# Optimization experiments

Hardware: AMD Instinct MI355X
Metric: run time of the kernel (lower is better)

## Reference

```python
import jax, jax.numpy as jnp
import numpy as np
import math

N_HEADS = 4
N_ITERS = 2  # SSFormer n=2; each loop iteration recomputes the same values (no feedback in the original code)
BN_EPS = 1e-5


def _attention(q, k, v):
    """SSTransformer: multi-head cross-attention over flattened spatial dims.
    q,k,v: [B, C, H, W] -> returns [B, C, L] with L = H*W.
    """
    b, c = q.shape[0], q.shape[1]
    L = q.shape[2] * q.shape[3]
    ch = c // N_HEADS
    scale = 1.0 / math.sqrt(math.sqrt(ch))
    qf = (q.reshape(b * N_HEADS, ch, L) * scale)
    kf = (k.reshape(b * N_HEADS, ch, L) * scale)
    vf = v.reshape(b * N_HEADS, ch, L)
    # weight: [B*H, t, s]
    w = jnp.einsum('bct,bcs->bts', qf, kf)
    w = jax.nn.softmax(w.astype(jnp.float32), axis=-1).astype(w.dtype)
    a = jnp.einsum('bts,bcs->bct', w, vf)
    return a.reshape(b, c, L)


def setup_inputs() -> dict:
    key = jax.random.key(0)
    k1, k2, k3, k4 = jax.random.split(key, 4)
    B, C, H, W = 8, 512, 32, 32
    c = jax.random.normal(k1, (B, C, H, W), dtype=jnp.float32)
    e = jax.random.normal(k2, (B, C, H, W), dtype=jnp.float32)
    conv_w = jax.random.normal(k3, (C, C, 1, 1), dtype=jnp.float32) / math.sqrt(C)
    conv_b = jax.random.normal(k4, (C,), dtype=jnp.float32) * 0.02
    bn_gamma = jnp.ones((C,), dtype=jnp.float32)
    bn_beta = jnp.zeros((C,), dtype=jnp.float32)
    return {"c": c, "e": e, "conv_w": conv_w, "conv_b": conv_b,
            "bn_gamma": bn_gamma, "bn_beta": bn_beta}


def reference(c, e, conv_w, conv_b, bn_gamma, bn_beta):
    bs, ch, h, w = c.shape
    L = h * w
    for _ in range(N_ITERS):
        _c = _attention(e, c, c)                       # [B, C, L]
        _e = _attention(_c.reshape(bs, ch, h, w), e, e)  # [B, C, L]
    _e = _e.reshape(bs, ch, h, w)
    # Proj: 1x1 conv + BatchNorm2d (training-mode batch stats) + Swish
    x = jnp.einsum('oc,bchw->bohw', conv_w.reshape(ch, ch), _e) + conv_b[None, :, None, None]
    mean = jnp.mean(x, axis=(0, 2, 3), keepdims=True)
    var = jnp.var(x, axis=(0, 2, 3), keepdims=True)
    xn = (x - mean) * jax.lax.rsqrt(var + BN_EPS)
    xn = xn * bn_gamma[None, :, None, None] + bn_beta[None, :, None, None]
    return xn * jax.nn.sigmoid(xn)
```

## Files before the change

### kernel.cpp

```cpp
#include <hip/hip_runtime.h>
#include <hip/hip_bf16.h>

typedef __attribute__((ext_vector_type(8))) short short8;
typedef __attribute__((ext_vector_type(4))) float floatx4;
typedef __attribute__((ext_vector_type(4))) float f32x4;
typedef __attribute__((ext_vector_type(16))) float f32x16;
typedef unsigned short u16;
typedef unsigned int u32;
typedef __attribute__((ext_vector_type(4))) unsigned int u32x4;
typedef __attribute__((ext_vector_type(8))) unsigned short ushort8;

#define LSEQ 1024
#define CHD  128
#define CEXP 0.12751744900425577f
#define THR_RAW 62.73318f

static __device__ __forceinline__ float b2f(u16 u) {
  union { u32 i; float f; } x; x.i = ((u32)u) << 16; return x.f;
}
static __device__ __forceinline__ u16 f2b(float f) {
  __hip_bfloat16 h = __float2bfloat16(f);
  return *reinterpret_cast<u16*>(&h);
}
static __device__ __forceinline__ u32 cvtpk(float a, float b) {
  u32 r;
  asm("v_cvt_pk_bf16_f32 %0, %1, %2" : "=v"(r) : "v"(a), "v"(b));
  return r;
}
static __device__ __forceinline__ void swap32(u32& a, u32& b) {
  asm("v_permlane32_swap_b32 %0, %1" : "+v"(a), "+v"(b));
}
static __device__ __forceinline__ short8 mk8(u32 a, u32 b, u32 c, u32 d) {
  union { u32x4 u; short8 s; } x;
  x.u[0] = a; x.u[1] = b; x.u[2] = c; x.u[3] = d;
  return x.s;
}
static __device__ __forceinline__ float exp2f_fast(float x) {
  float r;
  asm("v_exp_f32 %0, %1" : "=v"(r) : "v"(x));
  return r;
}
static __device__ __forceinline__ void gl_lds16(const void* g, void* l) {
  __builtin_amdgcn_global_load_lds((__attribute__((address_space(1))) const void*)g,
                                   (__attribute__((address_space(3))) void*)l, 16, 0, 0);
}
#define BARRIER() do { asm volatile("" ::: "memory"); __builtin_amdgcn_s_barrier(); asm volatile("" ::: "memory"); } while (0)
#define LGKM0()   do { asm volatile("s_waitcnt lgkmcnt(0)" ::: "memory"); __builtin_amdgcn_sched_barrier(0); } while (0)

__global__ __launch_bounds__(256) void k_prep(const float* __restrict__ cin,
                                              const float* __restrict__ ein,
                                              const float* __restrict__ Wf,
                                              u16* __restrict__ cV, u16* __restrict__ cT,
                                              u16* __restrict__ eV, u16* __restrict__ eT,
                                              u16* __restrict__ wb, float* __restrict__ zbuf) {
  __shared__ u16 tile[32][72];
  int z = blockIdx.z;
  int tid = threadIdx.x;
  if (z >= 64) {
    int wblk = (z - 64) * 64 + blockIdx.y * 16 + blockIdx.x;
    int base = (wblk * 256 + tid) * 8;
    f32x4 a = *(const f32x4*)(Wf + base);
    f32x4 b = *(const f32x4*)(Wf + base + 4);
    u32x4 u;
    u[0] = cvtpk(a[0], a[1]); u[1] = cvtpk(a[2], a[3]);
    u[2] = cvtpk(b[0], b[1]); u[3] = cvtpk(b[2], b[3]);
    *(u32x4*)(wb + base) = u;
    if (wblk == 0) {
      f32x4 zz; zz[0]=0.f; zz[1]=0.f; zz[2]=0.f; zz[3]=0.f;
      *(f32x4*)(zbuf + tid * 4) = zz;
    }
    return;
  }
  const float* in = (z < 32) ? cin : ein;
  u16* outV = (z < 32) ? cV : eV;
  u16* outT = (z < 32) ? cT : eT;
  int bh = z & 31, c0 = blockIdx.y * 32, s0 = blockIdx.x * 64;
  int cl = tid >> 3, sc = tid & 7;
  size_t off = ((size_t)bh * CHD + c0 + cl) * LSEQ + s0 + sc * 8;
  f32x4 a = *(const f32x4*)(in + off);
  f32x4 b = *(const f32x4*)(in + off + 4);
  u32x4 u;
  u[0] = cvtpk(a[0], a[1]); u[1] = cvtpk(a[2], a[3]);
  u[2] = cvtpk(b[0], b[1]); u[3] = cvtpk(b[2], b[3]);
  *(u32x4*)(outV + off) = u;
  *(u32x4*)&tile[cl][sc * 8] = u;
  __syncthreads();
  int sl = tid >> 2, cc = tid & 3;
  ushort8 v;
#pragma unroll
  for (int j = 0; j < 8; ++j) v[j] = tile[cc * 8 + j][sl];
  *(ushort8*)(outT + ((size_t)bh * LSEQ + s0 + sl) * CHD + c0 + cc * 8) = v;
}

__global__ __launch_bounds__(256, 2) void k_attn(const u16* __restrict__ eT,
                                                 const u16* __restrict__ cT,
                                                 const u16* __restrict__ cV,
                                                 const u16* __restrict__ eV,
                                                 u16* __restrict__ outT) {
  __shared__ char ldsbuf[66560];

  int bh = blockIdx.x, tt = blockIdx.y;
  int tid = threadIdx.x;
  int w = tid >> 6, lane = tid & 63;
  int tw = w & 1, sw = w >> 1;
  int ln = lane & 31, h = lane >> 5;
  int t0 = tt * 64 + tw * 32;

  float* bmbuf = (float*)(ldsbuf + 65536);
  float* lbuf  = (float*)(ldsbuf + 65536 + 512);

  auto stageK = [&](int buf, int sb, const char* kTb) {
#pragma unroll
    for (int it = 0; it < 4; ++it) {
      int bb = it * 4096 + tid * 16;
      int row = bb >> 8;
      int cb = (bb & 255) ^ ((row & 15) << 4);
      gl_lds16(kTb + (size_t)(sb * 64 + row) * 256 + cb, ldsbuf + buf * 16384 + bb);
    }
  };
  auto stageV = [&](int buf, int sb, const char* vb) {
#pragma unroll
    for (int it = 0; it < 4; ++it) {
      int bb = it * 4096 + tid * 16;
      int row = bb >> 7;
      int cb = (bb & 127) ^ ((row & 7) << 4);
      gl_lds16(vb + (size_t)row * 2048 + sb * 128 + cb, ldsbuf + 32768 + buf * 16384 + bb);
    }
  };

  short8 bq[8];
  f32x16 oacc[4];
  float m_r, l_r;
  int swz = (ln & 7) << 4;
  int kswz = (ln & 15) << 4;
  int krow = sw * 32 + ln;

  auto flash = [&](const char* kTb, const char* vb) {
    m_r = -1e30f; l_r = 0.f;
#pragma unroll
    for (int i = 0; i < 4; ++i)
#pragma unroll
      for (int r = 0; r < 16; ++r) oacc[i][r] = 0.f;

    stageK(0, 0, kTb); stageV(0, 0, vb);
    asm volatile("s_waitcnt vmcnt(0)" ::: "memory");
    BARRIER();

    for (int sb = 0; sb < 16; ++sb) {
      int cur = sb & 1;
      const char* K = ldsbuf + cur * 16384;
      const char* V = ldsbuf + 32768 + cur * 16384;
      f32x16 sa;
#pragma unroll
      for (int r = 0; r < 16; ++r) sa[r] = 0.f;

      if (sb < 15) stageK(cur ^ 1, sb + 1, kTb);
      short8 ka0 = *(const short8*)(K + krow * 256 + ((0  + h * 16) ^ kswz));
      short8 ka1 = *(const short8*)(K + krow * 256 + ((32 + h * 16) ^ kswz));
      short8 ka2 = *(const short8*)(K + krow * 256 + ((64 + h * 16) ^ kswz));
      short8 ka3 = *(const short8*)(K + krow * 256 + ((96 + h * 16) ^ kswz));
      BARRIER();
      LGKM0();
      __builtin_amdgcn_s_setprio(1);
      sa = __builtin_amdgcn_mfma_f32_32x32x16_bf16(ka0, bq[0], sa, 0, 0, 0);
      sa = __builtin_amdgcn_mfma_f32_32x32x16_bf16(ka1, bq[1], sa, 0, 0, 0);
      sa = __builtin_amdgcn_mfma_f32_32x32x16_bf16(ka2, bq[2], sa, 0, 0, 0);
      sa = __builtin_amdgcn_mfma_f32_32x32x16_bf16(ka3, bq[3], sa, 0, 0, 0);
      __builtin_amdgcn_s_setprio(0);
      BARRIER();

      if (sb < 15) stageV(cur ^ 1, sb + 1, vb);
      short8 kb0 = *(const short8*)(K + krow * 256 + ((128 + h * 16) ^ kswz));
      short8 kb1 = *(const short8*)(K + krow * 256 + ((160 + h * 16) ^ kswz));
      short8 kb2 = *(const short8*)(K + krow * 256 + ((192 + h * 16) ^ kswz));
      short8 kb3 = *(const short8*)(K + krow * 256 + ((224 + h * 16) ^ kswz));
      BARRIER();
      LGKM0();
      __builtin_amdgcn_s_setprio(1);
      sa = __builtin_amdgcn_mfma_f32_32x32x16_bf16(kb0, bq[4], sa, 0, 0, 0);
      sa = __builtin_amdgcn_mfma_f32_32x32x16_bf16(kb1, bq[5], sa, 0, 0, 0);
      sa = __builtin_amdgcn_mfma_f32_32x32x16_bf16(kb2, bq[6], sa, 0, 0, 0);
      sa = __builtin_amdgcn_mfma_f32_32x32x16_bf16(kb3, bq[7], sa, 0, 0, 0);
      __builtin_amdgcn_s_setprio(0);
      BARRIER();

      float bm = fmaxf(fmaxf(sa[0], sa[1]), fmaxf(sa[2], sa[3]));
      bm = fmaxf(bm, fmaxf(fmaxf(sa[4], sa[5]), fmaxf(sa[6], sa[7])));
      bm = fmaxf(bm, fmaxf(fmaxf(sa[8], sa[9]), fmaxf(sa[10], sa[11])));
      bm = fmaxf(bm, fmaxf(fmaxf(sa[12], sa[13]), fmaxf(sa[14], sa[15])));
      bm = fmaxf(bm, __shfl_xor(bm, 32));
      if (lane < 32) bmbuf[(tw * 2 + sw) * 32 + lane] = bm;
      LGKM0();
      BARRIER();
      bm = fmaxf(bm, bmbuf[(tw * 2 + (sw ^ 1)) * 32 + ln]);
      bool stay = __all(bm - m_r <= THR_RAW);
      if (!stay) {
        float mn = fmaxf(m_r, bm);
        float corr = exp2f_fast((m_r - mn) * CEXP);
        m_r = mn; l_r *= corr;
#pragma unroll
        for (int i = 0; i < 4; ++i)
#pragma unroll
          for (int r = 0; r < 16; ++r) oacc[i][r] *= corr;
      }
      float mnC = m_r * CEXP;
      float rs = 0.f;
#pragma unroll
      for (int r = 0; r < 16; ++r) {
        float p = exp2f_fast(__builtin_fmaf(sa[r], CEXP, -mnC));
        sa[r] = p; rs += p;
      }
      rs += __shfl_xor(rs, 32);
      l_r += rs;

      short8 bp0, bp1;
      {
        u32 w0 = cvtpk(sa[0], sa[1]),  w1 = cvtpk(sa[2], sa[3]);
        u32 w2 = cvtpk(sa[4], sa[5]),  w3 = cvtpk(sa[6], sa[7]);
        swap32(w0, w2); swap32(w1, w3);
        bp0 = mk8(w0, w1, w2, w3);
        u32 w4 = cvtpk(sa[8], sa[9]),  w5 = cvtpk(sa[10], sa[11]);
        u32 w6 = cvtpk(sa[12], sa[13]), w7 = cvtpk(sa[14], sa[15]);
        swap32(w4, w6); swap32(w5, w7);
        bp1 = mk8(w4, w5, w6, w7);
      }

      int vc0 = sw * 64 + h * 16;
      short8 va0 = *(const short8*)(V + (0  + ln) * 128 + (vc0 ^ swz));
      short8 va1 = *(const short8*)(V + (32 + ln) * 128 + (vc0 ^ swz));
      short8 va2 = *(const short8*)(V + (64 + ln) * 128 + (vc0 ^ swz));
      short8 va3 = *(const short8*)(V + (96 + ln) * 128 + (vc0 ^ swz));
      BARRIER();
      LGKM0();
      __builtin_amdgcn_s_setprio(1);
      oacc[0] = __builtin_amdgcn_mfma_f32_32x32x16_bf16(va0, bp0, oacc[0], 0, 0, 0);
      oacc[1] = __builtin_amdgcn_mfma_f32_32x32x16_bf16(va1, bp0, oacc[1], 0, 0, 0);
      oacc[2] = __builtin_amdgcn_mfma_f32_32x32x16_bf16(va2, bp0, oacc[2], 0, 0, 0);
      oacc[3] = __builtin_amdgcn_mfma_f32_32x32x16_bf16(va3, bp0, oacc[3], 0, 0, 0);
      __builtin_amdgcn_s_setprio(0);
      BARRIER();

      int vc1 = sw * 64 + 32 + h * 16;
      short8 vb0 = *(const short8*)(V + (0  + ln) * 128 + (vc1 ^ swz));
      short8 vb1 = *(const short8*)(V + (32 + ln) * 128 + (vc1 ^ swz));
      short8 vb2 = *(const short8*)(V + (64 + ln) * 128 + (vc1 ^ swz));
      short8 vb3 = *(const short8*)(V + (96 + ln) * 128 + (vc1 ^ swz));
      BARRIER();
      LGKM0();
      __builtin_amdgcn_s_setprio(1);
      oacc[0] = __builtin_amdgcn_mfma_f32_32x32x16_bf16(vb0, bp1, oacc[0], 0, 0, 0);
      oacc[1] = __builtin_amdgcn_mfma_f32_32x32x16_bf16(vb1, bp1, oacc[1], 0, 0, 0);
      oacc[2] = __builtin_amdgcn_mfma_f32_32x32x16_bf16(vb2, bp1, oacc[2], 0, 0, 0);
      oacc[3] = __builtin_amdgcn_mfma_f32_32x32x16_bf16(vb3, bp1, oacc[3], 0, 0, 0);
      __builtin_amdgcn_s_setprio(0);
      asm volatile("s_waitcnt vmcnt(0)" ::: "memory");
      BARRIER();
    }
  };

  auto merge_sw = [&]() {
    float* mb = (float*)(ldsbuf + 32768 + tw * 16384);
    if (sw == 1) {
#pragma unroll
      for (int i = 0; i < 4; ++i)
#pragma unroll
        for (int r = 0; r < 16; ++r) mb[(i * 16 + r) * 64 + lane] = oacc[i][r];
      if (lane < 32) lbuf[tw * 32 + lane] = l_r;
    }
    LGKM0();
    BARRIER();
    if (sw == 0) {
#pragma unroll
      for (int i = 0; i < 4; ++i)
#pragma unroll
        for (int r = 0; r < 16; ++r) oacc[i][r] += mb[(i * 16 + r) * 64 + lane];
      l_r += lbuf[tw * 32 + ln];
    }
  };

  const u16* qbase = eT + ((size_t)bh * LSEQ + t0 + ln) * CHD + h * 8;
#pragma unroll
  for (int k = 0; k < 8; ++k) bq[k] = *(const short8*)(qbase + k * 16);

  flash((const char*)(cT + (size_t)bh * LSEQ * CHD),
        (const char*)(cV + (size_t)bh * CHD * LSEQ));

  merge_sw();
  if (sw == 0) {
    float inv = 1.0f / l_r;
    char* qt = ldsbuf + tw * 8192;
#pragma unroll
    for (int m = 0; m < 4; ++m)
#pragma unroll
      for (int q = 0; q < 8; ++q) {
        u32 pk = cvtpk(oacc[m][2 * q] * inv, oacc[m][2 * q + 1] * inv);
        int c2 = m * 64 + 4 * (q & 1) + 16 * (q >> 1) + 8 * h;
        *(u32*)(qt + ln * 256 + (c2 ^ swz)) = pk;
      }
  }
  LGKM0();
  BARRIER();
  {
    const char* qt = ldsbuf + tw * 8192;
#pragma unroll
    for (int k = 0; k < 8; ++k)
      bq[k] = *(const short8*)(qt + ln * 256 + ((k * 32 + h * 16) ^ swz));
  }
  LGKM0();
  BARRIER();

  flash((const char*)(eT + (size_t)bh * LSEQ * CHD),
        (const char*)(eV + (size_t)bh * CHD * LSEQ));

  merge_sw();
  BARRIER();
  if (sw == 0) {
    float inv = 1.0f / l_r;
    char* ot = ldsbuf + tw * 8192;
#pragma unroll
    for (int m = 0; m < 4; ++m)
#pragma unroll
      for (int q = 0; q < 8; ++q) {
        u32 pk = cvtpk(oacc[m][2 * q] * inv, oacc[m][2 * q + 1] * inv);
        int c2 = m * 64 + 4 * (q & 1) + 16 * (q >> 1) + 8 * h;
        *(u32*)(ot + ln * 256 + (c2 ^ swz)) = pk;
      }
    asm volatile("" ::: "memory");
    u16* orow = outT + ((size_t)bh * LSEQ + t0 + ln) * CHD;
#pragma unroll
    for (int it = 0; it < 8; ++it) {
      int col = h * 128 + it * 16;
      ushort8 d = *(const ushort8*)(ot + ln * 256 + (col ^ swz));
      *(ushort8*)((char*)orow + col) = d;
    }
  }
}

__global__ __launch_bounds__(256) void k_proj(const u16* __restrict__ Wm,
                                              const u16* __restrict__ eT,
                                              const float* __restrict__ bias,
                                              u16* __restrict__ x,
                                              float* __restrict__ chsum,
                                              float* __restrict__ chsq) {
  __shared__ char lds[65536];
  int lt = blockIdx.x, ot = blockIdx.y;
  int b = lt >> 3;
  int l0b = (lt & 7) * 128;
  int o0 = ot * 128;
  int tid = threadIdx.x, w = tid >> 6, lane = tid & 63, lo = lane & 15, hi = lane >> 4;
  int wm = w >> 1, wn = w & 1;
  const char* Wb = (const char*)Wm;
  const char* eTb = (const char*)eT;

  auto stageA = [&](int buf, int kb) {
    char* dst = lds + buf * 16384;
#pragma unroll
    for (int it = 0; it < 4; ++it) {
      int bb = it * 4096 + tid * 16;
      int row = bb >> 7;
      int cb = (bb & 127) ^ ((row & 7) << 4);
      gl_lds16(Wb + (size_t)(o0 + row) * 1024 + kb * 128 + cb, dst + bb);
    }
  };
  auto stageB = [&](int buf, int kb) {
    char* dst = lds + 32768 + buf * 16384;
    int page = b * 4 + (kb >> 1);
    int choff = (kb & 1) * 128;
#pragma unroll
    for (int it = 0; it < 4; ++it) {
      int bb = it * 4096 + tid * 16;
      int row = bb >> 7;
      int cb = (bb & 127) ^ ((row & 7) << 4);
      gl_lds16(eTb + ((size_t)page * 1024 + l0b + row) * 256 + choff + cb, dst + bb);
    }
  };

  floatx4 acc[4][4];
#pragma unroll
  for (int i = 0; i < 4; ++i)
#pragma unroll
    for (int j = 0; j < 4; ++j) { acc[i][j][0]=0.f; acc[i][j][1]=0.f; acc[i][j][2]=0.f; acc[i][j][3]=0.f; }

  stageA(0, 0); stageB(0, 0);

  for (int kb = 0; kb < 8; ++kb) {
    int cur = kb & 1;
    __builtin_amdgcn_s_barrier();
    if (kb < 7) { stageA(cur ^ 1, kb + 1); stageB(cur ^ 1, kb + 1); }
    if (kb < 7) { asm volatile("s_waitcnt vmcnt(8)" ::: "memory"); }
    else        { asm volatile("s_waitcnt vmcnt(0)" ::: "memory"); }
    __builtin_amdgcn_s_barrier();
    const char* A = lds + cur * 16384;
    const char* B = lds + 32768 + cur * 16384;
#pragma unroll
    for (int kk = 0; kk < 2; ++kk) {
      short8 af[4], bf[4];
#pragma unroll
      for (int mi = 0; mi < 4; ++mi) {
        int row = wm * 64 + mi * 16 + lo;
        af[mi] = *(const short8*)(A + row * 128 + ((kk * 64 + hi * 16) ^ ((row & 7) << 4)));
      }
#pragma unroll
      for (int ni = 0; ni < 4; ++ni) {
        int row = wn * 64 + ni * 16 + lo;
        bf[ni] = *(const short8*)(B + row * 128 + ((kk * 64 + hi * 16) ^ ((row & 7) << 4)));
      }
      __builtin_amdgcn_s_setprio(1);
#pragma unroll
      for (int mi = 0; mi < 4; ++mi)
#pragma unroll
        for (int ni = 0; ni < 4; ++ni)
          acc[mi][ni] = __builtin_amdgcn_mfma_f32_16x16x32_bf16(af[mi], bf[ni], acc[mi][ni], 0, 0, 0);
      __builtin_amdgcn_s_setprio(0);
    }
  }

#pragma unroll
  for (int mi = 0; mi < 4; ++mi) {
#pragma unroll
    for (int r = 0; r < 4; ++r) {
      int o = o0 + wm * 64 + mi * 16 + hi * 4 + r;
      float bv = bias[o];
      float s = 0.f, q = 0.f;
#pragma unroll
      for (int ni = 0; ni < 4; ++ni) {
        float xv = acc[mi][ni][r] + bv;
        x[((size_t)b * 512 + o) * LSEQ + l0b + wn * 64 + ni * 16 + lo] = f2b(xv);
        s += xv; q += xv * xv;
      }
#pragma unroll
      for (int d = 1; d < 16; d <<= 1) { s += __shfl_xor(s, d); q += __shfl_xor(q, d); }
      if (lo == 0) {
        atomicAdd(&chsum[o], s);
        atomicAdd(&chsq[o], q);
      }
    }
  }
}

__global__ __launch_bounds__(256) void k_final(const u16* __restrict__ x,
                                               const float* __restrict__ chsum,
                                               const float* __restrict__ chsq,
                                               const float* __restrict__ gamma,
                                               const float* __restrict__ beta,
                                               float* __restrict__ out) {
  int idx = blockIdx.x * 256 + threadIdx.x;
  int base = idx * 8;
  int ch = (base >> 10) & 511;
  const float invn = 1.0f / 8192.0f;
  float mean = chsum[ch] * invn;
  float var = chsq[ch] * invn - mean * mean;
  float rstd = rsqrtf(var + 1e-5f);
  float sc = gamma[ch] * rstd;
  float sh = beta[ch] - mean * sc;
  ushort8 vx = *(const ushort8*)(x + base);
  f32x4 o0, o1;
#pragma unroll
  for (int j = 0; j < 8; ++j) {
    float xn = b2f(vx[j]) * sc + sh;
    float sg = 1.0f / (1.0f + __expf(-xn));
    float r = xn * sg;
    if (j < 4) o0[j] = r; else o1[j - 4] = r;
  }
  *(f32x4*)(out + base) = o0;
  *(f32x4*)(out + base + 4) = o1;
}

extern "C" void kernel_launch(void* const* d_in, const int* in_sizes, int n_in,
                              void* d_out, int out_size, void* d_ws, size_t ws_size,
                              hipStream_t stream) {
  const float* c     = (const float*)d_in[0];
  const float* e     = (const float*)d_in[1];
  const float* Wf    = (const float*)d_in[2];
  const float* bias  = (const float*)d_in[3];
  const float* gamma = (const float*)d_in[4];
  const float* beta  = (const float*)d_in[5];
  float* outp = (float*)d_out;

  char* ws = (char*)d_ws;
  const size_t TB = (size_t)32 * 1024 * 128 * 2;
  u16* eT  = (u16*)(ws);
  u16* cT  = (u16*)(ws + TB);
  u16* cV  = (u16*)(ws + 2 * TB);
  u16* eV  = (u16*)(ws + 3 * TB);
  u16* xT  = (u16*)(ws + 4 * TB);
  u16* Wbf = (u16*)(ws + 5 * TB);
  float* chsum = (float*)(ws + 5 * TB + (1 << 20));
  float* chsq  = chsum + 512;
  u16* x   = (u16*)(ws + 6 * TB);

  dim3 tb(256);

  k_prep<<<dim3(16, 4, 66), tb, 0, stream>>>(c, e, Wf, cV, cT, eV, eT, Wbf, chsum);
  k_attn<<<dim3(32, 16), tb, 0, stream>>>(eT, cT, cV, eV, xT);
  k_proj<<<dim3(64, 4), tb, 0, stream>>>(Wbf, xT, bias, x, chsum, chsq);
  k_final<<<dim3(2048), tb, 0, stream>>>(x, chsum, chsq, gamma, beta, outp);
}
```

Baseline: 106.2 us.

## Decouple split-KV waves with independent softmax max and merge-time rescale

The per-block cross-wave max exchange through LDS is removed. Each s-split wave now keeps its own running max, and the two partial results are merged once at the end with exp-based rescaling. The K/V staging is restructured into one barrier pair per block, prefetching both next tiles together with a partial vmcnt wait. All K and V fragments are loaded up front, and the QK^T MFMA chain is split into two independent accumulators to shorten dependency chains. This removes many barriers per iteration, in exchange for more live registers and a slightly more complex final merge.

```diff
diff --git a/kernel.cpp b/kernel.cpp
--- a/kernel.cpp
+++ b/kernel.cpp
@@ -45,7 +45,7 @@
                                    (__attribute__((address_space(3))) void*)l, 16, 0, 0);
 }
 #define BARRIER() do { asm volatile("" ::: "memory"); __builtin_amdgcn_s_barrier(); asm volatile("" ::: "memory"); } while (0)
-#define LGKM0()   do { asm volatile("s_waitcnt lgkmcnt(0)" ::: "memory"); __builtin_amdgcn_sched_barrier(0); } while (0)
+#define LGKM0()   do { asm volatile("s_waitcnt lgkmcnt(0)" ::: "memory"); } while (0)
 
 __global__ __launch_bounds__(256) void k_prep(const float* __restrict__ cin,
                                               const float* __restrict__ ein,
@@ -106,9 +106,6 @@
   int ln = lane & 31, h = lane >> 5;
   int t0 = tt * 64 + tw * 32;
 
-  float* bmbuf = (float*)(ldsbuf + 65536);
-  float* lbuf  = (float*)(ldsbuf + 65536 + 512);
-
   auto stageK = [&](int buf, int sb, const char* kTb) {
 #pragma unroll
     for (int it = 0; it < 4; ++it) {
@@ -143,56 +140,52 @@
       for (int r = 0; r < 16; ++r) oacc[i][r] = 0.f;
 
     stageK(0, 0, kTb); stageV(0, 0, vb);
-    asm volatile("s_waitcnt vmcnt(0)" ::: "memory");
-    BARRIER();
 
     for (int sb = 0; sb < 16; ++sb) {
       int cur = sb & 1;
+      BARRIER();
+      if (sb < 15) { stageK(cur ^ 1, sb + 1, kTb); stageV(cur ^ 1, sb + 1, vb); }
+      if (sb < 15) { asm volatile("s_waitcnt vmcnt(8)" ::: "memory"); }
+      else         { asm volatile("s_waitcnt vmcnt(0)" ::: "memory"); }
+      BARRIER();
+
       const char* K = ldsbuf + cur * 16384;
       const char* V = ldsbuf + 32768 + cur * 16384;
+
+      short8 kf[8], vf0[4], vf1[4];
+#pragma unroll
+      for (int k = 0; k < 8; ++k)
+        kf[k] = *(const short8*)(K + krow * 256 + ((k * 32 + h * 16) ^ kswz));
+      int vc0 = sw * 64 + h * 16, vc1 = sw * 64 + 32 + h * 16;
+#pragma unroll
+      for (int m = 0; m < 4; ++m) {
+        vf0[m] = *(const short8*)(V + (m * 32 + ln) * 128 + (vc0 ^ swz));
+        vf1[m] = *(const short8*)(V + (m * 32 + ln) * 128 + (vc1 ^ swz));
+      }
+
+      f32x16 saA, saB;
+#pragma unroll
+      for (int r = 0; r < 16; ++r) { saA[r] = 0.f; saB[r] = 0.f; }
+      __builtin_amdgcn_s_setprio(1);
+      saA = __builtin_amdgcn_mfma_f32_32x32x16_bf16(kf[0], bq[0], saA, 0, 0, 0);
+      saB = __builtin_amdgcn_mfma_f32_32x32x16_bf16(kf[4], bq[4], saB, 0, 0, 0);
+      saA = __builtin_amdgcn_mfma_f32_32x32x16_bf16(kf[1], bq[1], saA, 0, 0, 0);
+      saB = __builtin_amdgcn_mfma_f32_32x32x16_bf16(kf[5], bq[5], saB, 0, 0, 0);
+      saA = __builtin_amdgcn_mfma_f32_32x32x16_bf16(kf[2], bq[2], saA, 0, 0, 0);
+      saB = __builtin_amdgcn_mfma_f32_32x32x16_bf16(kf[6], bq[6], saB, 0, 0, 0);
+      saA = __builtin_amdgcn_mfma_f32_32x32x16_bf16(kf[3], bq[3], saA, 0, 0, 0);
+      saB = __builtin_amdgcn_mfma_f32_32x32x16_bf16(kf[7], bq[7], saB, 0, 0, 0);
+      __builtin_amdgcn_s_setprio(0);
+
       f32x16 sa;
 #pragma unroll
-      for (int r = 0; r < 16; ++r) sa[r] = 0.f;
-
-      if (sb < 15) stageK(cur ^ 1, sb + 1, kTb);
-      short8 ka0 = *(const short8*)(K + krow * 256 + ((0  + h * 16) ^ kswz));
-      short8 ka1 = *(const short8*)(K + krow * 256 + ((32 + h * 16) ^ kswz));
-      short8 ka2 = *(const short8*)(K + krow * 256 + ((64 + h * 16) ^ kswz));
-      short8 ka3 = *(const short8*)(K + krow * 256 + ((96 + h * 16) ^ kswz));
-      BARRIER();
-      LGKM0();
-      __builtin_amdgcn_s_setprio(1);
-      sa = __builtin_amdgcn_mfma_f32_32x32x16_bf16(ka0, bq[0], sa, 0, 0, 0);
-      sa = __builtin_amdgcn_mfma_f32_32x32x16_bf16(ka1, bq[1], sa, 0, 0, 0);
-      sa = __builtin_amdgcn_mfma_f32_32x32x16_bf16(ka2, bq[2], sa, 0, 0, 0);
-      sa = __builtin_amdgcn_mfma_f32_32x32x16_bf16(ka3, bq[3], sa, 0, 0, 0);
-      __builtin_amdgcn_s_setprio(0);
-      BARRIER();
-
-      if (sb < 15) stageV(cur ^ 1, sb + 1, vb);
-      short8 kb0 = *(const short8*)(K + krow * 256 + ((128 + h * 16) ^ kswz));
-      short8 kb1 = *(const short8*)(K + krow * 256 + ((160 + h * 16) ^ kswz));
-      short8 kb2 = *(const short8*)(K + krow * 256 + ((192 + h * 16) ^ kswz));
-      short8 kb3 = *(const short8*)(K + krow * 256 + ((224 + h * 16) ^ kswz));
-      BARRIER();
-      LGKM0();
-      __builtin_amdgcn_s_setprio(1);
-      sa = __builtin_amdgcn_mfma_f32_32x32x16_bf16(kb0, bq[4], sa, 0, 0, 0);
-      sa = __builtin_amdgcn_mfma_f32_32x32x16_bf16(kb1, bq[5], sa, 0, 0, 0);
-      sa = __builtin_amdgcn_mfma_f32_32x32x16_bf16(kb2, bq[6], sa, 0, 0, 0);
-      sa = __builtin_amdgcn_mfma_f32_32x32x16_bf16(kb3, bq[7], sa, 0, 0, 0);
-      __builtin_amdgcn_s_setprio(0);
-      BARRIER();
+      for (int r = 0; r < 16; ++r) sa[r] = saA[r] + saB[r];
 
       float bm = fmaxf(fmaxf(sa[0], sa[1]), fmaxf(sa[2], sa[3]));
       bm = fmaxf(bm, fmaxf(fmaxf(sa[4], sa[5]), fmaxf(sa[6], sa[7])));
       bm = fmaxf(bm, fmaxf(fmaxf(sa[8], sa[9]), fmaxf(sa[10], sa[11])));
       bm = fmaxf(bm, fmaxf(fmaxf(sa[12], sa[13]), fmaxf(sa[14], sa[15])));
       bm = fmaxf(bm, __shfl_xor(bm, 32));
-      if (lane < 32) bmbuf[(tw * 2 + sw) * 32 + lane] = bm;
-      LGKM0();
-      BARRIER();
-      bm = fmaxf(bm, bmbuf[(tw * 2 + (sw ^ 1)) * 32 + ln]);
       bool stay = __all(bm - m_r <= THR_RAW);
       if (!stay) {
         float mn = fmaxf(m_r, bm);
@@ -225,56 +218,48 @@
         bp1 = mk8(w4, w5, w6, w7);
       }
 
-      int vc0 = sw * 64 + h * 16;
-      short8 va0 = *(const short8*)(V + (0  + ln) * 128 + (vc0 ^ swz));
-      short8 va1 = *(const short8*)(V + (32 + ln) * 128 + (vc0 ^ swz));
-      short8 va2 = *(const short8*)(V + (64 + ln) * 128 + (vc0 ^ swz));
-      short8 va3 = *(const short8*)(V + (96 + ln) * 128 + (vc0 ^ swz));
-      BARRIER();
-      LGKM0();
       __builtin_amdgcn_s_setprio(1);
-      oacc[0] = __builtin_amdgcn_mfma_f32_32x32x16_bf16(va0, bp0, oacc[0], 0, 0, 0);
-      oacc[1] = __builtin_amdgcn_mfma_f32_32x32x16_bf16(va1, bp0, oacc[1], 0, 0, 0);
-      oacc[2] = __builtin_amdgcn_mfma_f32_32x32x16_bf16(va2, bp0, oacc[2], 0, 0, 0);
-      oacc[3] = __builtin_amdgcn_mfma_f32_32x32x16_bf16(va3, bp0, oacc[3], 0, 0, 0);
+      oacc[0] = __builtin_amdgcn_mfma_f32_32x32x16_bf16(vf0[0], bp0, oacc[0], 0, 0, 0);
+      oacc[1] = __builtin_amdgcn_mfma_f32_32x32x16_bf16(vf0[1], bp0, oacc[1], 0, 0, 0);
+      oacc[2] = __builtin_amdgcn_mfma_f32_32x32x16_bf16(vf0[2], bp0, oacc[2], 0, 0, 0);
+      oacc[3] = __builtin_amdgcn_mfma_f32_32x32x16_bf16(vf0[3], bp0, oacc[3], 0, 0, 0);
+      oacc[0] = __builtin_amdgcn_mfma_f32_32x32x16_bf16(vf1[0], bp1, oacc[0], 0, 0, 0);
+      oacc[1] = __builtin_amdgcn_mfma_f32_32x32x16_bf16(vf1[1], bp1, oacc[1], 0, 0, 0);
+      oacc[2] = __builtin_amdgcn_mfma_f32_32x32x16_bf16(vf1[2], bp1, oacc[2], 0, 0, 0);
+      oacc[3] = __builtin_amdgcn_mfma_f32_32x32x16_bf16(vf1[3], bp1, oacc[3], 0, 0, 0);
       __builtin_amdgcn_s_setprio(0);
-      BARRIER();
-
-      int vc1 = sw * 64 + 32 + h * 16;
-      short8 vb0 = *(const short8*)(V + (0  + ln) * 128 + (vc1 ^ swz));
-      short8 vb1 = *(const short8*)(V + (32 + ln) * 128 + (vc1 ^ swz));
-      short8 vb2 = *(const short8*)(V + (64 + ln) * 128 + (vc1 ^ swz));
-      short8 vb3 = *(const short8*)(V + (96 + ln) * 128 + (vc1 ^ swz));
-      BARRIER();
-      LGKM0();
-      __builtin_amdgcn_s_setprio(1);
-      oacc[0] = __builtin_amdgcn_mfma_f32_32x32x16_bf16(vb0, bp1, oacc[0], 0, 0, 0);
-      oacc[1] = __builtin_amdgcn_mfma_f32_32x32x16_bf16(vb1, bp1, oacc[1], 0, 0, 0);
-      oacc[2] = __builtin_amdgcn_mfma_f32_32x32x16_bf16(vb2, bp1, oacc[2], 0, 0, 0);
-      oacc[3] = __builtin_amdgcn_mfma_f32_32x32x16_bf16(vb3, bp1, oacc[3], 0, 0, 0);
-      __builtin_amdgcn_s_setprio(0);
-      asm volatile("s_waitcnt vmcnt(0)" ::: "memory");
-      BARRIER();
     }
   };
 
   auto merge_sw = [&]() {
-    float* mb = (float*)(ldsbuf + 32768 + tw * 16384);
+    BARRIER();
+    float* mO  = (float*)(ldsbuf + 32768 + tw * 16384);
+    float* mml = (float*)(ldsbuf + 65536) + tw * 64;
     if (sw == 1) {
 #pragma unroll
       for (int i = 0; i < 4; ++i)
 #pragma unroll
-        for (int r = 0; r < 16; ++r) mb[(i * 16 + r) * 64 + lane] = oacc[i][r];
-      if (lane < 32) lbuf[tw * 32 + lane] = l_r;
+        for (int r = 0; r < 16; ++r) {
+          int c_idx = i * 32 + (r & 3) + 8 * (r >> 2) + 4 * h;
+          mO[c_idx * 32 + ln] = oacc[i][r];
+        }
+      if (lane < 32) { mml[lane] = m_r; mml[32 + lane] = l_r; }
     }
     LGKM0();
     BARRIER();
     if (sw == 0) {
+      float m1 = mml[ln], l1 = mml[32 + ln];
+      float m = fmaxf(m_r, m1);
+      float e0 = exp2f_fast((m_r - m) * CEXP);
+      float e1 = exp2f_fast((m1 - m) * CEXP);
+      l_r = l_r * e0 + l1 * e1;
 #pragma unroll
       for (int i = 0; i < 4; ++i)
 #pragma unroll
-        for (int r = 0; r < 16; ++r) oacc[i][r] += mb[(i * 16 + r) * 64 + lane];
-      l_r += lbuf[tw * 32 + ln];
+        for (int r = 0; r < 16; ++r) {
+          int c_idx = i * 32 + (r & 3) + 8 * (r >> 2) + 4 * h;
+          oacc[i][r] = oacc[i][r] * e0 + mO[c_idx * 32 + ln] * e1;
+        }
     }
   };
 
@@ -284,8 +269,8 @@
 
   flash((const char*)(cT + (size_t)bh * LSEQ * CHD),
         (const char*)(cV + (size_t)bh * CHD * LSEQ));
-
   merge_sw();
+
   if (sw == 0) {
     float inv = 1.0f / l_r;
     char* qt = ldsbuf + tw * 8192;
@@ -311,9 +296,8 @@
 
   flash((const char*)(eT + (size_t)bh * LSEQ * CHD),
         (const char*)(eV + (size_t)bh * CHD * LSEQ));
-
   merge_sw();
-  BARRIER();
+
   if (sw == 0) {
     float inv = 1.0f / l_r;
     char* ot = ldsbuf + tw * 8192;
```

Result: no change. 108.3 us (+1.9%).
